# Kernel optimization log

Hardware: AMD Instinct MI355X
Metric: run time of the kernel (lower is better)

Reference implementation:

```python
import jax, jax.numpy as jnp
import numpy as np

B, S, D, H, DK, DV = 4, 1024, 1024, 16, 64, 64
NEG = -1e9  # matches torch masked_fill(-1000000000.0)


def setup_inputs() -> dict:
    key = jax.random.key(0)
    ks = jax.random.split(key, 12)
    scale = 1.0 / np.sqrt(D)
    return {
        "querys": jax.random.normal(ks[0], (B, S, D), jnp.float32),
        "keys": jax.random.normal(ks[1], (B, S, D), jnp.float32),
        "values": jax.random.normal(ks[2], (B, S, D), jnp.float32),
        "mask": jax.random.randint(ks[3], (S, S), 0, 2, jnp.int32),
        # stacked per-head projection params (nn.Linear style: y = x @ W^T + b -> here W stored as [D, dk])
        "Wq": jax.random.normal(ks[4], (H, D, DK), jnp.float32) * scale,
        "bq": jax.random.normal(ks[5], (H, DK), jnp.float32) * 0.01,
        "Wk": jax.random.normal(ks[6], (H, D, DK), jnp.float32) * scale,
        "bk": jax.random.normal(ks[7], (H, DK), jnp.float32) * 0.01,
        "Wv": jax.random.normal(ks[8], (H, D, DV), jnp.float32) * scale,
        "bv": jax.random.normal(ks[9], (H, DV), jnp.float32) * 0.01,
        "Wp": jax.random.normal(ks[10], (H * DV, D), jnp.float32) * (1.0 / np.sqrt(H * DV)),
        "bp": jax.random.normal(ks[11], (D,), jnp.float32) * 0.01,
    }


def reference(querys, keys, values, mask, Wq, bq, Wk, bk, Wv, bv, Wp, bp):
    # per-head projections, all heads batched: [B, H, S, dk/dv]
    q = jnp.einsum('bsd,hdk->bhsk', querys, Wq) + bq[None, :, None, :]
    k = jnp.einsum('bsd,hdk->bhsk', keys, Wk) + bk[None, :, None, :]
    v = jnp.einsum('bsd,hdv->bhsv', values, Wv) + bv[None, :, None, :]
    # scores: NO 1/sqrt(dk) scaling, faithful to original broadcast multiply+sum
    scores = jnp.einsum('bhqd,bhkd->bhqk', q, k)  # [B, H, S, S]
    scores = jnp.where(mask[None, None, :, :] == 0, NEG, scores)
    w = jax.nn.softmax(scores, axis=-1)
    o = jnp.einsum('bhqk,bhkv->bhqv', w, v)        # [B, H, S, dv]
    # concat heads along feature dim (head order = H axis), then project
    o = o.transpose(0, 2, 1, 3).reshape(B, S, H * DV)
    return o @ Wp + bp
```

## Files before the change

kernel.cpp:

```cpp
#include <hip/hip_runtime.h>
#include <hip/hip_bf16.h>

typedef unsigned short u16;
typedef unsigned long long u64;
typedef __attribute__((ext_vector_type(4))) float f32x4;
typedef __attribute__((ext_vector_type(8))) __bf16 bf16x8;
typedef __attribute__((ext_vector_type(8))) u16 u16x8;

#define DEV __device__ __forceinline__
#define MFMA(a, b, c) __builtin_amdgcn_mfma_f32_16x16x32_bf16(a, b, c, 0, 0, 0)


DEV u16 f2bf(float x) {
  unsigned u = __builtin_bit_cast(unsigned, x);
  u += 0x7fffu + ((u >> 16) & 1u);
  return (u16)(u >> 16);
}
DEV float bf2f(u16 h) {
  unsigned u = ((unsigned)h) << 16;
  return __builtin_bit_cast(float, u);
}
DEV bf16x8 frag8(const u16* p) {
  return __builtin_bit_cast(bf16x8, *(const u16x8*)p);
}
DEV void gload16(u16* lds, const u16* g) {
  __builtin_amdgcn_global_load_lds((const __attribute__((address_space(1))) void*)g,
                                   (__attribute__((address_space(3))) void*)lds, 16, 0, 0);
}

__global__ __launch_bounds__(256) void prep_weights(
    const float* __restrict__ Wq, const float* __restrict__ Wk,
    const float* __restrict__ Wv, const float* __restrict__ Wp,
    u16* __restrict__ wqh, u16* __restrict__ wql,
    u16* __restrict__ wkh, u16* __restrict__ wkl,
    u16* __restrict__ wvh, u16* __restrict__ wph) {
  __shared__ float tile[64][65];
  const int k0 = blockIdx.x * 64;
  const int h = blockIdx.y;
  const int z = blockIdx.z;
  const float* src;
  u16* dhi;
  u16* dlo = nullptr;
  int hs, rs;
  if (z == 0)      { src = Wq; dhi = wqh; dlo = wql; hs = 65536; rs = 64; }
  else if (z == 1) { src = Wk; dhi = wkh; dlo = wkl; hs = 65536; rs = 64; }
  else if (z == 2) { src = Wv; dhi = wvh;            hs = 65536; rs = 64; }
  else             { src = Wp; dhi = wph;            hs = 64;    rs = 1024; }
  const int t = threadIdx.x;
#pragma unroll
  for (int i = 0; i < 16; ++i) {
    int kk = i * 4 + (t >> 6), nn = t & 63;
    tile[kk][nn] = src[h * hs + (k0 + kk) * rs + nn];
  }
  __syncthreads();
#pragma unroll
  for (int i = 0; i < 16; ++i) {
    int nn = i * 4 + (t >> 6), kk = t & 63;
    float x = tile[kk][nn];
    u16 hi = f2bf(x);
    int idx = (h * 64 + nn) * 1024 + k0 + kk;
    dhi[idx] = hi;
    if (dlo) dlo[idx] = f2bf(x - bf2f(hi));
  }
}

__global__ __launch_bounds__(256) void pack_mask(const int* __restrict__ mask,
                                                 u64* __restrict__ mp) {
  int g = blockIdx.x * 4 + (threadIdx.x >> 6);
  int lane = threadIdx.x & 63;
  int v = mask[(g >> 4) * 1024 + (g & 15) * 64 + lane];
  u64 bits = __ballot(v != 0);
  if (lane == 0) mp[g] = bits;
}

__global__ __launch_bounds__(256) void split_x(
    const float* __restrict__ q, const float* __restrict__ k,
    const float* __restrict__ v, u16* __restrict__ qh, u16* __restrict__ ql,
    u16* __restrict__ kh, u16* __restrict__ kl, u16* __restrict__ vh) {
  const int z = blockIdx.y;
  const float* src = (z == 0) ? q : (z == 1) ? k : v;
  u16* dh = (z == 0) ? qh : (z == 1) ? kh : vh;
  u16* dl = (z == 0) ? ql : kl;
  const bool split = (z < 2);
  const long base = (long)(blockIdx.x * 256 + threadIdx.x) * 8;
  f32x4 v0 = *(const f32x4*)&src[base];
  f32x4 v1 = *(const f32x4*)&src[base + 4];
  u16x8 hi, lo;
#pragma unroll
  for (int e = 0; e < 4; ++e) {
    u16 h0 = f2bf(v0[e]), h1 = f2bf(v1[e]);
    hi[e] = h0;
    hi[4 + e] = h1;
    lo[e] = f2bf(v0[e] - bf2f(h0));
    lo[4 + e] = f2bf(v1[e] - bf2f(h1));
  }
  *(u16x8*)&dh[base] = hi;
  if (split) *(u16x8*)&dl[base] = lo;
}

__global__ __launch_bounds__(256, 3) void proj_fused(
    const u16* __restrict__ Xqh, const u16* __restrict__ Xql,
    const u16* __restrict__ Xkh, const u16* __restrict__ Xkl,
    const u16* __restrict__ Xvh, const u16* __restrict__ wqh,
    const u16* __restrict__ wql, const u16* __restrict__ wkh,
    const u16* __restrict__ wkl, const u16* __restrict__ wvh,
    const float* __restrict__ bq, const float* __restrict__ bk,
    const float* __restrict__ bv, u16* __restrict__ Qh, u16* __restrict__ Ql,
    u16* __restrict__ Kh, u16* __restrict__ Kl, u16* __restrict__ Vt) {
  __shared__ alignas(16) u16 Ah[128 * 32];
  __shared__ alignas(16) u16 Al[128 * 32];
  __shared__ alignas(16) u16 Bh[128 * 32];
  __shared__ alignas(16) u16 Bl[128 * 32];
  const int z = blockIdx.z;
  const bool split = (z < 2);
  const u16* Ah_src = (z == 0) ? Xqh : (z == 1) ? Xkh : Xvh;
  const u16* Al_src = (z == 0) ? Xql : Xkl;
  const u16* Bh_src = (z == 0) ? wqh : (z == 1) ? wkh : wvh;
  const u16* Bl_src = (z == 0) ? wql : wkl;
  const float* bias = (z == 0) ? bq : (z == 1) ? bk : bv;
  u16* Oh = (z == 0) ? Qh : (z == 1) ? Kh : Vt;
  u16* Ol = (z == 0) ? Ql : Kl;

  const int m0 = blockIdx.x * 128, n0 = blockIdx.y * 128;
  const int t = threadIdx.x, w = t >> 6, l = t & 63;
  const int wr = w >> 1, wc = w & 1, lr = l & 15, lq = l >> 4;
  const int srow = l >> 2, scol = (l & 3) * 8;
  f32x4 acc[4][4];
#pragma unroll
  for (int i = 0; i < 4; ++i)
#pragma unroll
    for (int j = 0; j < 4; ++j) acc[i][j] = (f32x4){0.f, 0.f, 0.f, 0.f};

  for (int ks = 0; ks < 32; ++ks) {
    const int k0 = ks * 32;
#pragma unroll
    for (int i = 0; i < 2; ++i) {
      const int ci = w * 2 + i;
      const int rr = ci * 16 + srow;
      gload16(&Ah[ci * 512], &Ah_src[(m0 + rr) * 1024 + k0 + scol]);
      gload16(&Bh[ci * 512], &Bh_src[(n0 + rr) * 1024 + k0 + scol]);
      if (split) {
        gload16(&Al[ci * 512], &Al_src[(m0 + rr) * 1024 + k0 + scol]);
        gload16(&Bl[ci * 512], &Bl_src[(n0 + rr) * 1024 + k0 + scol]);
      }
    }
    __syncthreads();
    bf16x8 ah[4], al[4];
#pragma unroll
    for (int mi = 0; mi < 4; ++mi) {
      int row = wr * 64 + mi * 16 + lr;
      ah[mi] = frag8(&Ah[row * 32 + lq * 8]);
      if (split) al[mi] = frag8(&Al[row * 32 + lq * 8]);
    }
    if (split) {
#pragma unroll
      for (int nj = 0; nj < 4; ++nj) {
        int col = wc * 64 + nj * 16 + lr;
        bf16x8 bh = frag8(&Bh[col * 32 + lq * 8]);
        bf16x8 bl = frag8(&Bl[col * 32 + lq * 8]);
#pragma unroll
        for (int mi = 0; mi < 4; ++mi) {
          acc[mi][nj] = MFMA(ah[mi], bh, acc[mi][nj]);
          acc[mi][nj] = MFMA(ah[mi], bl, acc[mi][nj]);
          acc[mi][nj] = MFMA(al[mi], bh, acc[mi][nj]);
        }
      }
    } else {
#pragma unroll
      for (int nj = 0; nj < 4; ++nj) {
        int col = wc * 64 + nj * 16 + lr;
        bf16x8 bh = frag8(&Bh[col * 32 + lq * 8]);
#pragma unroll
        for (int mi = 0; mi < 4; ++mi) acc[mi][nj] = MFMA(ah[mi], bh, acc[mi][nj]);
      }
    }
    __syncthreads();
  }
#pragma unroll
  for (int nj = 0; nj < 4; ++nj) {
    int n = n0 + wc * 64 + nj * 16 + lr;
    float bb = bias[n];
    int h = n >> 6, dk = n & 63;
#pragma unroll
    for (int mi = 0; mi < 4; ++mi) {
#pragma unroll
      for (int j = 0; j < 4; ++j) {
        int m = m0 + wr * 64 + mi * 16 + lq * 4 + j;
        int b = m >> 10, s = m & 1023;
        float x = acc[mi][nj][j] + bb;
        if (split) {
          int idx = ((b * 16 + h) * 1024 + s) * 64 + dk;
          u16 hh = f2bf(x);
          Oh[idx] = hh;
          Ol[idx] = f2bf(x - bf2f(hh));
        } else {
          int idx = ((b * 16 + h) * 64 + dk) * 1024 + s;
          Oh[idx] = f2bf(x);
        }
      }
    }
  }
}

__global__ __launch_bounds__(256, 2) void attn_kernel(
    const u16* __restrict__ Qh, const u16* __restrict__ Ql,
    const u16* __restrict__ Kh, const u16* __restrict__ Kl,
    const u16* __restrict__ Vt, const u64* __restrict__ mp,
    u16* __restrict__ Oc) {
  __shared__ alignas(16) u16 Ks_h[64 * 72];
  __shared__ alignas(16) u16 Ks_l[64 * 72];
  __shared__ alignas(16) u16 Vs[64 * 72];
  __shared__ alignas(16) u16 Ps[4][16 * 72];
  __shared__ u64 mw[64];
  const int bid = blockIdx.x;
  const int bh = bid >> 4, qt = bid & 15, q0 = qt * 64;
  const int t = threadIdx.x, w = t >> 6, l = t & 63;
  const int lr = l & 15, lq = l >> 4;
  const int qrow = q0 + w * 16 + lr;
  const int rr = t >> 2, c0 = (t & 3) * 8;

  bf16x8 qh[2], qlo[2];
#pragma unroll
  for (int d = 0; d < 2; ++d) {
    int off = (bh * 1024 + qrow) * 64 + d * 32 + lq * 8;
    qh[d] = frag8(&Qh[off]);
    qlo[d] = frag8(&Ql[off]);
  }
  f32x4 o[4];
#pragma unroll
  for (int dv = 0; dv < 4; ++dv) o[dv] = (f32x4){0.f, 0.f, 0.f, 0.f};
  float mr[4] = {-1e30f, -1e30f, -1e30f, -1e30f};
  float lsum[4] = {0.f, 0.f, 0.f, 0.f};

  u16x8 rKh[2], rKl[2], rVs[2];
  u64 rMw = 0;
  auto issue = [&](int kt) {
    const int k0 = kt * 64;
#pragma unroll
    for (int half = 0; half < 2; ++half) {
      int c = c0 + half * 32;
      rKh[half] = *(const u16x8*)&Kh[(bh * 1024 + k0 + rr) * 64 + c];
      rKl[half] = *(const u16x8*)&Kl[(bh * 1024 + k0 + rr) * 64 + c];
      rVs[half] = *(const u16x8*)&Vt[(bh * 64 + rr) * 1024 + k0 + c];
    }
    if (t < 64) rMw = mp[(q0 + t) * 16 + kt];
  };

  issue(0);
  for (int kt = 0; kt < 16; ++kt) {
#pragma unroll
    for (int half = 0; half < 2; ++half) {
      int c = c0 + half * 32;
      *(u16x8*)&Ks_h[rr * 72 + c] = rKh[half];
      *(u16x8*)&Ks_l[rr * 72 + c] = rKl[half];
      *(u16x8*)&Vs[rr * 72 + c] = rVs[half];
    }
    if (t < 64) mw[t] = rMw;
    __syncthreads();
    if (kt < 15) issue(kt + 1);
    f32x4 s[4];
#pragma unroll
    for (int kb = 0; kb < 4; ++kb) {
      f32x4 a = (f32x4){0.f, 0.f, 0.f, 0.f};
#pragma unroll
      for (int d = 0; d < 2; ++d) {
        bf16x8 kfh = frag8(&Ks_h[(kb * 16 + lr) * 72 + d * 32 + lq * 8]);
        bf16x8 kfl = frag8(&Ks_l[(kb * 16 + lr) * 72 + d * 32 + lq * 8]);
        a = MFMA(qh[d], kfh, a);
        a = MFMA(qh[d], kfl, a);
        a = MFMA(qlo[d], kfh, a);
      }
      s[kb] = a;
    }
#pragma unroll
    for (int j = 0; j < 4; ++j) {
      u64 word = mw[w * 16 + lq * 4 + j];
      float mx = -3e38f;
#pragma unroll
      for (int kb = 0; kb < 4; ++kb) {
        float v = s[kb][j];
        if (!((word >> (kb * 16 + lr)) & 1ull)) v = -1e9f;
        s[kb][j] = v;
        mx = fmaxf(mx, v);
      }
#pragma unroll
      for (int mk = 1; mk < 16; mk <<= 1) mx = fmaxf(mx, __shfl_xor(mx, mk));
      float mn = fmaxf(mr[j], mx);
      float scale = __expf(mr[j] - mn);
      mr[j] = mn;
      float ps = 0.f;
#pragma unroll
      for (int kb = 0; kb < 4; ++kb) {
        float p = __expf(s[kb][j] - mn);
        s[kb][j] = p;
        ps += p;
      }
#pragma unroll
      for (int mk = 1; mk < 16; mk <<= 1) ps += __shfl_xor(ps, mk);
      lsum[j] = lsum[j] * scale + ps;
#pragma unroll
      for (int dv = 0; dv < 4; ++dv) o[dv][j] *= scale;
    }
    u16* pw = &Ps[w][0];
#pragma unroll
    for (int j = 0; j < 4; ++j)
#pragma unroll
      for (int kb = 0; kb < 4; ++kb)
        pw[(lq * 4 + j) * 72 + kb * 16 + lr] = f2bf(s[kb][j]);
#pragma unroll
    for (int kk = 0; kk < 2; ++kk) {
      bf16x8 pa = frag8(&pw[lr * 72 + kk * 32 + lq * 8]);
#pragma unroll
      for (int dv = 0; dv < 4; ++dv) {
        bf16x8 vf = frag8(&Vs[(dv * 16 + lr) * 72 + kk * 32 + lq * 8]);
        o[dv] = MFMA(pa, vf, o[dv]);
      }
    }
    __syncthreads();
  }
  const int b = bh >> 4, h = bh & 15;
#pragma unroll
  for (int j = 0; j < 4; ++j) {
    float inv = 1.f / lsum[j];
    int srow = q0 + w * 16 + lq * 4 + j;
    int base = (b * 1024 + srow) * 1024 + h * 64;
#pragma unroll
    for (int dv = 0; dv < 4; ++dv) Oc[base + dv * 16 + lr] = f2bf(o[dv][j] * inv);
  }
}

__global__ __launch_bounds__(256) void final_kernel(
    const u16* __restrict__ A, const u16* __restrict__ Bt,
    const float* __restrict__ bias, float* __restrict__ out) {
  __shared__ alignas(16) u16 As[64 * 32];
  __shared__ alignas(16) u16 Bs[128 * 32];
  const int m0 = blockIdx.x * 64, n0 = blockIdx.y * 128;
  const int t = threadIdx.x, w = t >> 6, l = t & 63;
  const int wr = w >> 1, wc = w & 1, lr = l & 15, lq = l >> 4;
  const int srow = l >> 2, scol = (l & 3) * 8;
  f32x4 acc[2][4];
#pragma unroll
  for (int i = 0; i < 2; ++i)
#pragma unroll
    for (int j = 0; j < 4; ++j) acc[i][j] = (f32x4){0.f, 0.f, 0.f, 0.f};

  for (int ks = 0; ks < 32; ++ks) {
    const int k0 = ks * 32;
    gload16(&As[w * 512], &A[(m0 + w * 16 + srow) * 1024 + k0 + scol]);
#pragma unroll
    for (int i = 0; i < 2; ++i) {
      const int ci = w * 2 + i;
      gload16(&Bs[ci * 512], &Bt[(n0 + ci * 16 + srow) * 1024 + k0 + scol]);
    }
    __syncthreads();
    bf16x8 a[2];
#pragma unroll
    for (int mi = 0; mi < 2; ++mi)
      a[mi] = frag8(&As[(wr * 32 + mi * 16 + lr) * 32 + lq * 8]);
#pragma unroll
    for (int nj = 0; nj < 4; ++nj) {
      bf16x8 bfr = frag8(&Bs[(wc * 64 + nj * 16 + lr) * 32 + lq * 8]);
#pragma unroll
      for (int mi = 0; mi < 2; ++mi) acc[mi][nj] = MFMA(a[mi], bfr, acc[mi][nj]);
    }
    __syncthreads();
  }
#pragma unroll
  for (int nj = 0; nj < 4; ++nj) {
    int n = n0 + wc * 64 + nj * 16 + lr;
    float bb = bias[n];
#pragma unroll
    for (int mi = 0; mi < 2; ++mi)
#pragma unroll
      for (int j = 0; j < 4; ++j) {
        int m = m0 + wr * 32 + mi * 16 + lq * 4 + j;
        out[m * 1024 + n] = acc[mi][nj][j] + bb;
      }
  }
}

extern "C" void kernel_launch(void* const* d_in, const int* in_sizes, int n_in,
                              void* d_out, int out_size, void* d_ws, size_t ws_size,
                              hipStream_t stream) {
  (void)in_sizes; (void)n_in; (void)out_size; (void)ws_size;
  const float* querys = (const float*)d_in[0];
  const float* keys = (const float*)d_in[1];
  const float* values = (const float*)d_in[2];
  const int* mask = (const int*)d_in[3];
  const float* Wq = (const float*)d_in[4];
  const float* bq = (const float*)d_in[5];
  const float* Wk = (const float*)d_in[6];
  const float* bk = (const float*)d_in[7];
  const float* Wv = (const float*)d_in[8];
  const float* bv = (const float*)d_in[9];
  const float* Wp = (const float*)d_in[10];
  const float* bp = (const float*)d_in[11];
  float* out = (float*)d_out;

  char* ws = (char*)d_ws;
  const size_t MB = 1024ull * 1024ull;
  u16* Qh = (u16*)(ws + 0 * MB);
  u16* Ql = (u16*)(ws + 8 * MB);
  u16* Kh = (u16*)(ws + 16 * MB);
  u16* Kl = (u16*)(ws + 24 * MB);
  u16* Vt = (u16*)(ws + 32 * MB);
  u16* Oc = (u16*)(ws + 40 * MB);
  u16* wqh = (u16*)(ws + 48 * MB);
  u16* wql = (u16*)(ws + 50 * MB);
  u16* wkh = (u16*)(ws + 52 * MB);
  u16* wkl = (u16*)(ws + 54 * MB);
  u16* wvh = (u16*)(ws + 56 * MB);
  u16* wph = (u16*)(ws + 58 * MB);
  u16* Xkl = (u16*)(ws + 60 * MB);
  u16* Xvh = (u16*)(ws + 68 * MB);
  u64* mp = (u64*)(ws + 76 * MB);
  u16* Xqh = (u16*)d_out;
  u16* Xql = (u16*)((char*)d_out + 8 * MB);
  u16* Xkh = Oc;

  prep_weights<<<dim3(16, 16, 4), 256, 0, stream>>>(Wq, Wk, Wv, Wp, wqh, wql, wkh,
                                                    wkl, wvh, wph);
  pack_mask<<<dim3(4096), 256, 0, stream>>>(mask, mp);
  split_x<<<dim3(2048, 3), 256, 0, stream>>>(querys, keys, values, Xqh, Xql, Xkh,
                                             Xkl, Xvh);
  proj_fused<<<dim3(32, 8, 3), 256, 0, stream>>>(Xqh, Xql, Xkh, Xkl, Xvh, wqh, wql,
                                                 wkh, wkl, wvh, bq, bk, bv, Qh, Ql,
                                                 Kh, Kl, Vt);
  attn_kernel<<<dim3(1024), 256, 0, stream>>>(Qh, Ql, Kh, Kl, Vt, mp, Oc);
  final_kernel<<<dim3(64, 8), 256, 0, stream>>>(Oc, wph, bp, out);
}
```

Baseline: 318.2 us.

## Pre-expand mask into additive fragment layout and use exp2 softmax with lazy rescale

```diff
diff --git a/kernel.cpp b/kernel.cpp
--- a/kernel.cpp
+++ b/kernel.cpp
@@ -1,5 +1,6 @@
 #include <hip/hip_runtime.h>
 #include <hip/hip_bf16.h>
+#include <math.h>
 
 typedef unsigned short u16;
 typedef unsigned long long u64;
@@ -64,15 +65,6 @@
   }
 }
 
-__global__ __launch_bounds__(256) void pack_mask(const int* __restrict__ mask,
-                                                 u64* __restrict__ mp) {
-  int g = blockIdx.x * 4 + (threadIdx.x >> 6);
-  int lane = threadIdx.x & 63;
-  int v = mask[(g >> 4) * 1024 + (g & 15) * 64 + lane];
-  u64 bits = __ballot(v != 0);
-  if (lane == 0) mp[g] = bits;
-}
-
 __global__ __launch_bounds__(256) void split_x(
     const float* __restrict__ q, const float* __restrict__ k,
     const float* __restrict__ v, u16* __restrict__ qh, u16* __restrict__ ql,
@@ -96,6 +88,23 @@
   }
   *(u16x8*)&dh[base] = hi;
   if (split) *(u16x8*)&dl[base] = lo;
+}
+
+__global__ __launch_bounds__(256) void expand_mask(const int* __restrict__ mask,
+                                                   float* __restrict__ Mexp) {
+  const int gid = blockIdx.x * 256 + threadIdx.x;
+  const int qb = gid >> 10, kt = (gid >> 6) & 15, l = gid & 63;
+  const int qbase = qb * 16 + (l >> 4) * 4;
+  const int kbase = kt * 64 + (l & 15);
+  float* dst = &Mexp[(size_t)gid * 16];
+#pragma unroll
+  for (int kb = 0; kb < 4; ++kb) {
+    f32x4 v;
+#pragma unroll
+    for (int j = 0; j < 4; ++j)
+      v[j] = (mask[(qbase + j) * 1024 + kbase + kb * 16] == 0) ? -1e9f : 0.f;
+    *(f32x4*)&dst[kb * 4] = v;
+  }
 }
 
 __global__ __launch_bounds__(256, 3) void proj_fused(
@@ -176,6 +185,7 @@
     }
     __syncthreads();
   }
+  const float escale = (z == 0) ? 1.4426950408889634f : 1.0f;
 #pragma unroll
   for (int nj = 0; nj < 4; ++nj) {
     int n = n0 + wc * 64 + nj * 16 + lr;
@@ -187,7 +197,7 @@
       for (int j = 0; j < 4; ++j) {
         int m = m0 + wr * 64 + mi * 16 + lq * 4 + j;
         int b = m >> 10, s = m & 1023;
-        float x = acc[mi][nj][j] + bb;
+        float x = (acc[mi][nj][j] + bb) * escale;
         if (split) {
           int idx = ((b * 16 + h) * 1024 + s) * 64 + dk;
           u16 hh = f2bf(x);
@@ -202,22 +212,22 @@
   }
 }
 
-__global__ __launch_bounds__(256, 2) void attn_kernel(
+__global__ __launch_bounds__(256, 3) void attn_kernel(
     const u16* __restrict__ Qh, const u16* __restrict__ Ql,
     const u16* __restrict__ Kh, const u16* __restrict__ Kl,
-    const u16* __restrict__ Vt, const u64* __restrict__ mp,
+    const u16* __restrict__ Vt, const float* __restrict__ Mexp,
     u16* __restrict__ Oc) {
   __shared__ alignas(16) u16 Ks_h[64 * 72];
   __shared__ alignas(16) u16 Ks_l[64 * 72];
   __shared__ alignas(16) u16 Vs[64 * 72];
   __shared__ alignas(16) u16 Ps[4][16 * 72];
-  __shared__ u64 mw[64];
   const int bid = blockIdx.x;
   const int bh = bid >> 4, qt = bid & 15, q0 = qt * 64;
   const int t = threadIdx.x, w = t >> 6, l = t & 63;
   const int lr = l & 15, lq = l >> 4;
   const int qrow = q0 + w * 16 + lr;
   const int rr = t >> 2, c0 = (t & 3) * 8;
+  const float* mbase = &Mexp[(size_t)((qt * 4 + w) * 16) * 1024 + l * 16];
 
   bf16x8 qh[2], qlo[2];
 #pragma unroll
@@ -233,7 +243,7 @@
   float lsum[4] = {0.f, 0.f, 0.f, 0.f};
 
   u16x8 rKh[2], rKl[2], rVs[2];
-  u64 rMw = 0;
+  f32x4 rM[4];
   auto issue = [&](int kt) {
     const int k0 = kt * 64;
 #pragma unroll
@@ -243,7 +253,9 @@
       rKl[half] = *(const u16x8*)&Kl[(bh * 1024 + k0 + rr) * 64 + c];
       rVs[half] = *(const u16x8*)&Vt[(bh * 64 + rr) * 1024 + k0 + c];
     }
-    if (t < 64) rMw = mp[(q0 + t) * 16 + kt];
+#pragma unroll
+    for (int kb = 0; kb < 4; ++kb)
+      rM[kb] = *(const f32x4*)&mbase[kt * 1024 + kb * 4];
   };
 
   issue(0);
@@ -255,13 +267,14 @@
       *(u16x8*)&Ks_l[rr * 72 + c] = rKl[half];
       *(u16x8*)&Vs[rr * 72 + c] = rVs[half];
     }
-    if (t < 64) mw[t] = rMw;
+    f32x4 s[4];
+#pragma unroll
+    for (int kb = 0; kb < 4; ++kb) s[kb] = rM[kb];
     __syncthreads();
     if (kt < 15) issue(kt + 1);
-    f32x4 s[4];
 #pragma unroll
     for (int kb = 0; kb < 4; ++kb) {
-      f32x4 a = (f32x4){0.f, 0.f, 0.f, 0.f};
+      f32x4 a = s[kb];
 #pragma unroll
       for (int d = 0; d < 2; ++d) {
         bf16x8 kfh = frag8(&Ks_h[(kb * 16 + lr) * 72 + d * 32 + lq * 8]);
@@ -274,32 +287,26 @@
     }
 #pragma unroll
     for (int j = 0; j < 4; ++j) {
-      u64 word = mw[w * 16 + lq * 4 + j];
-      float mx = -3e38f;
+      float mx = fmaxf(fmaxf(s[0][j], s[1][j]), fmaxf(s[2][j], s[3][j]));
+#pragma unroll
+      for (int mk = 1; mk < 16; mk <<= 1) mx = fmaxf(mx, __shfl_xor(mx, mk));
+      if (mx > mr[j]) {
+        float scale = exp2f(mr[j] - mx);
+        mr[j] = mx;
+        lsum[j] *= scale;
+#pragma unroll
+        for (int dv = 0; dv < 4; ++dv) o[dv][j] *= scale;
+      }
+      float ps = 0.f;
 #pragma unroll
       for (int kb = 0; kb < 4; ++kb) {
-        float v = s[kb][j];
-        if (!((word >> (kb * 16 + lr)) & 1ull)) v = -1e9f;
-        s[kb][j] = v;
-        mx = fmaxf(mx, v);
-      }
-#pragma unroll
-      for (int mk = 1; mk < 16; mk <<= 1) mx = fmaxf(mx, __shfl_xor(mx, mk));
-      float mn = fmaxf(mr[j], mx);
-      float scale = __expf(mr[j] - mn);
-      mr[j] = mn;
-      float ps = 0.f;
-#pragma unroll
-      for (int kb = 0; kb < 4; ++kb) {
-        float p = __expf(s[kb][j] - mn);
+        float p = exp2f(s[kb][j] - mr[j]);
         s[kb][j] = p;
         ps += p;
       }
 #pragma unroll
       for (int mk = 1; mk < 16; mk <<= 1) ps += __shfl_xor(ps, mk);
-      lsum[j] = lsum[j] * scale + ps;
-#pragma unroll
-      for (int dv = 0; dv < 4; ++dv) o[dv][j] *= scale;
+      lsum[j] += ps;
     }
     u16* pw = &Ps[w][0];
 #pragma unroll
@@ -413,19 +420,19 @@
   u16* wph = (u16*)(ws + 58 * MB);
   u16* Xkl = (u16*)(ws + 60 * MB);
   u16* Xvh = (u16*)(ws + 68 * MB);
-  u64* mp = (u64*)(ws + 76 * MB);
   u16* Xqh = (u16*)d_out;
   u16* Xql = (u16*)((char*)d_out + 8 * MB);
   u16* Xkh = Oc;
+  float* Mexp = (float*)(ws + 48 * MB);
 
   prep_weights<<<dim3(16, 16, 4), 256, 0, stream>>>(Wq, Wk, Wv, Wp, wqh, wql, wkh,
                                                     wkl, wvh, wph);
-  pack_mask<<<dim3(4096), 256, 0, stream>>>(mask, mp);
   split_x<<<dim3(2048, 3), 256, 0, stream>>>(querys, keys, values, Xqh, Xql, Xkh,
                                              Xkl, Xvh);
   proj_fused<<<dim3(32, 8, 3), 256, 0, stream>>>(Xqh, Xql, Xkh, Xkl, Xvh, wqh, wql,
                                                  wkh, wkl, wvh, bq, bk, bv, Qh, Ql,
                                                  Kh, Kl, Vt);
-  attn_kernel<<<dim3(1024), 256, 0, stream>>>(Qh, Ql, Kh, Kl, Vt, mp, Oc);
+  expand_mask<<<dim3(256), 256, 0, stream>>>(mask, Mexp);
+  attn_kernel<<<dim3(1024), 256, 0, stream>>>(Qh, Ql, Kh, Kl, Vt, Mexp, Oc);
   final_kernel<<<dim3(64, 8), 256, 0, stream>>>(Oc, wph, bp, out);
 }
```

Result: slower. 337.5 us (+6.1%).

## Enlarge attention blocks to 128 query rows and use exp2 softmax with lazy rescale

Applied to the files above, without the earlier changes.

```diff
diff --git a/kernel.cpp b/kernel.cpp
--- a/kernel.cpp
+++ b/kernel.cpp
@@ -1,5 +1,6 @@
 #include <hip/hip_runtime.h>
 #include <hip/hip_bf16.h>
+#include <math.h>
 
 typedef unsigned short u16;
 typedef unsigned long long u64;
@@ -176,6 +177,7 @@
     }
     __syncthreads();
   }
+  const float escale = (z == 0) ? 1.4426950408889634f : 1.0f;
 #pragma unroll
   for (int nj = 0; nj < 4; ++nj) {
     int n = n0 + wc * 64 + nj * 16 + lr;
@@ -187,7 +189,7 @@
       for (int j = 0; j < 4; ++j) {
         int m = m0 + wr * 64 + mi * 16 + lq * 4 + j;
         int b = m >> 10, s = m & 1023;
-        float x = acc[mi][nj][j] + bb;
+        float x = (acc[mi][nj][j] + bb) * escale;
         if (split) {
           int idx = ((b * 16 + h) * 1024 + s) * 64 + dk;
           u16 hh = f2bf(x);
@@ -202,7 +204,7 @@
   }
 }
 
-__global__ __launch_bounds__(256, 2) void attn_kernel(
+__global__ __launch_bounds__(512, 4) void attn_kernel(
     const u16* __restrict__ Qh, const u16* __restrict__ Ql,
     const u16* __restrict__ Kh, const u16* __restrict__ Kl,
     const u16* __restrict__ Vt, const u64* __restrict__ mp,
@@ -210,14 +212,14 @@
   __shared__ alignas(16) u16 Ks_h[64 * 72];
   __shared__ alignas(16) u16 Ks_l[64 * 72];
   __shared__ alignas(16) u16 Vs[64 * 72];
-  __shared__ alignas(16) u16 Ps[4][16 * 72];
-  __shared__ u64 mw[64];
+  __shared__ alignas(16) u16 Ps[8][16 * 72];
+  __shared__ u64 mw[128];
   const int bid = blockIdx.x;
-  const int bh = bid >> 4, qt = bid & 15, q0 = qt * 64;
+  const int bh = bid & 63, qt = bid >> 6, q0 = qt * 128;
   const int t = threadIdx.x, w = t >> 6, l = t & 63;
   const int lr = l & 15, lq = l >> 4;
   const int qrow = q0 + w * 16 + lr;
-  const int rr = t >> 2, c0 = (t & 3) * 8;
+  const int rr = t >> 3, c0 = (t & 7) * 8;
 
   bf16x8 qh[2], qlo[2];
 #pragma unroll
@@ -232,30 +234,22 @@
   float mr[4] = {-1e30f, -1e30f, -1e30f, -1e30f};
   float lsum[4] = {0.f, 0.f, 0.f, 0.f};
 
-  u16x8 rKh[2], rKl[2], rVs[2];
+  u16x8 rKh, rKl, rVs;
   u64 rMw = 0;
   auto issue = [&](int kt) {
     const int k0 = kt * 64;
-#pragma unroll
-    for (int half = 0; half < 2; ++half) {
-      int c = c0 + half * 32;
-      rKh[half] = *(const u16x8*)&Kh[(bh * 1024 + k0 + rr) * 64 + c];
-      rKl[half] = *(const u16x8*)&Kl[(bh * 1024 + k0 + rr) * 64 + c];
-      rVs[half] = *(const u16x8*)&Vt[(bh * 64 + rr) * 1024 + k0 + c];
-    }
-    if (t < 64) rMw = mp[(q0 + t) * 16 + kt];
+    rKh = *(const u16x8*)&Kh[(bh * 1024 + k0 + rr) * 64 + c0];
+    rKl = *(const u16x8*)&Kl[(bh * 1024 + k0 + rr) * 64 + c0];
+    rVs = *(const u16x8*)&Vt[(bh * 64 + rr) * 1024 + k0 + c0];
+    if (t < 128) rMw = mp[(q0 + t) * 16 + kt];
   };
 
   issue(0);
   for (int kt = 0; kt < 16; ++kt) {
-#pragma unroll
-    for (int half = 0; half < 2; ++half) {
-      int c = c0 + half * 32;
-      *(u16x8*)&Ks_h[rr * 72 + c] = rKh[half];
-      *(u16x8*)&Ks_l[rr * 72 + c] = rKl[half];
-      *(u16x8*)&Vs[rr * 72 + c] = rVs[half];
-    }
-    if (t < 64) mw[t] = rMw;
+    *(u16x8*)&Ks_h[rr * 72 + c0] = rKh;
+    *(u16x8*)&Ks_l[rr * 72 + c0] = rKl;
+    *(u16x8*)&Vs[rr * 72 + c0] = rVs;
+    if (t < 128) mw[t] = rMw;
     __syncthreads();
     if (kt < 15) issue(kt + 1);
     f32x4 s[4];
@@ -285,21 +279,23 @@
       }
 #pragma unroll
       for (int mk = 1; mk < 16; mk <<= 1) mx = fmaxf(mx, __shfl_xor(mx, mk));
-      float mn = fmaxf(mr[j], mx);
-      float scale = __expf(mr[j] - mn);
-      mr[j] = mn;
+      if (mx > mr[j]) {
+        float scale = exp2f(mr[j] - mx);
+        mr[j] = mx;
+        lsum[j] *= scale;
+#pragma unroll
+        for (int dv = 0; dv < 4; ++dv) o[dv][j] *= scale;
+      }
       float ps = 0.f;
 #pragma unroll
       for (int kb = 0; kb < 4; ++kb) {
-        float p = __expf(s[kb][j] - mn);
+        float p = exp2f(s[kb][j] - mr[j]);
         s[kb][j] = p;
         ps += p;
       }
 #pragma unroll
       for (int mk = 1; mk < 16; mk <<= 1) ps += __shfl_xor(ps, mk);
-      lsum[j] = lsum[j] * scale + ps;
-#pragma unroll
-      for (int dv = 0; dv < 4; ++dv) o[dv][j] *= scale;
+      lsum[j] += ps;
     }
     u16* pw = &Ps[w][0];
 #pragma unroll
@@ -426,6 +422,6 @@
   proj_fused<<<dim3(32, 8, 3), 256, 0, stream>>>(Xqh, Xql, Xkh, Xkl, Xvh, wqh, wql,
                                                  wkh, wkl, wvh, bq, bk, bv, Qh, Ql,
                                                  Kh, Kl, Vt);
-  attn_kernel<<<dim3(1024), 256, 0, stream>>>(Qh, Ql, Kh, Kl, Vt, mp, Oc);
+  attn_kernel<<<dim3(512), 512, 0, stream>>>(Qh, Ql, Kh, Kl, Vt, mp, Oc);
   final_kernel<<<dim3(64, 8), 256, 0, stream>>>(Oc, wph, bp, out);
 }
```

Result: slower. 383.1 us (+20.4%).
